# Kernel tuning notes

Measured on AMD Instinct MI355X. Metric: run time of the kernel, lower is better.

The kernel has to match this reference:

```python
import jax, jax.numpy as jnp
import numpy as np
from jax import lax

B, L, V, E, F, C, K = 8, 2500, 50000, 100, 50, 8921, 10
PAD = K // 2  # padding=floor(filter_size/2) -> output length L+1 for even K


def setup_inputs() -> dict:
    key = jax.random.key(0)
    ks = jax.random.split(key, 7)
    text = jax.random.randint(ks[0], (B, L), 0, V, dtype=jnp.int32)
    embed_weight = jax.random.normal(ks[1], (V, E), jnp.float32) * 0.1
    embed_weight = embed_weight.at[0].set(0.0)  # padding_idx=0
    conv_w = jax.random.normal(ks[2], (F, E, K), jnp.float32) * (2.0 / (E * K + F)) ** 0.5
    conv_b = jnp.zeros((F,), jnp.float32)
    Q_w = jax.random.normal(ks[3], (C, F), jnp.float32) * (2.0 / (C + F)) ** 0.5
    out_w = jax.random.normal(ks[4], (C, F), jnp.float32) * (2.0 / (C + F)) ** 0.5
    out_b = jnp.zeros((C,), jnp.float32)
    return {"text": text, "embed_weight": embed_weight, "conv_w": conv_w,
            "conv_b": conv_b, "Q_w": Q_w, "out_w": out_w, "out_b": out_b}


def reference(text, embed_weight, conv_w, conv_b, Q_w, out_w, out_b):
    # Embedding lookup (dropout omitted: eval mode): (B, L, E)
    x = embed_weight[text]
    # Conv1d over length: torch Conv1d(E, F, K, padding=PAD)
    x = jnp.transpose(x, (0, 2, 1))  # (B, E, L)
    z = lax.conv_general_dilated(x, conv_w, window_strides=(1,),
                                 padding=[(PAD, PAD)],
                                 dimension_numbers=("NCH", "OIH", "NCH"))
    z = z + conv_b[None, :, None]
    Z = jnp.tanh(jnp.transpose(z, (0, 2, 1)))  # (B, L', F), L' = L+1
    # Per-label attention: Q_w (C,F) @ Z^T -> (B, C, L'), softmax over length
    scores = jnp.einsum("cf,blf->bcl", Q_w, Z)
    alpha = jax.nn.softmax(scores, axis=2)  # (B, C, L')
    # Attention-weighted sum: (B, C, F)
    Ecf = jnp.einsum("bcl,blf->bcf", alpha, Z)
    # Per-class dot-product readout
    logits = jnp.sum(out_w[None] * Ecf, axis=2) + out_b  # (B, C)
    return logits, alpha
```

## Files before the change

### kernel.cpp

```cpp
#include <hip/hip_runtime.h>
#include <math.h>

#define BB 8
#define LL 2500
#define VV 50000
#define EE 100
#define FF 50
#define CC 8921
#define KK 10
#define PADW 5
#define LOUT 2501
#define NLT 157
#define LPAD (NLT * 16)
#define NCT 140
#define NT16 (NCT * 4)
#define NG 10

typedef __attribute__((ext_vector_type(8))) short bf16x8;
typedef __attribute__((ext_vector_type(4))) float f32x4;

__device__ __forceinline__ short to_bf16(float f) {
  unsigned u = __builtin_bit_cast(unsigned, f);
  u += 0x7FFFu + ((u >> 16) & 1u);
  return (short)(u >> 16);
}

__global__ void k1_conv(const int* __restrict__ text,
                        const float* __restrict__ embed,
                        const float* __restrict__ convw,
                        const float* __restrict__ convb,
                        short* __restrict__ Zp) {
  __shared__ float xw[73 * 101];
  __shared__ short zt[64][72];
  const int b   = blockIdx.y;
  const int l0  = blockIdx.x * 64;
  const int tid = threadIdx.x;

  for (int i = tid; i < 64 * 72 / 2; i += 256) ((int*)zt)[i] = 0;

  for (int idx = tid; idx < 73 * 100; idx += 256) {
    int r = idx / 100;
    int e = idx - r * 100;
    int t = l0 - PADW + r;
    float v = 0.f;
    if (t >= 0 && t < LL) {
      int tok = text[b * LL + t];
      v = embed[tok * EE + e];
    }
    xw[r * 101 + e] = v;
  }
  __syncthreads();

  const int ll = tid & 63;
  const int fg = __builtin_amdgcn_readfirstlane(tid >> 6);
  const int l  = l0 + ll;

  float acc[13];
#pragma unroll
  for (int j = 0; j < 13; ++j) {
    int f = fg + 4 * j;
    acc[j] = (f < FF) ? convb[f] : 0.f;
  }

  for (int e = 0; e < EE; ++e) {
    float xk[KK];
#pragma unroll
    for (int k = 0; k < KK; ++k) xk[k] = xw[(ll + k) * 101 + e];
#pragma unroll
    for (int j = 0; j < 13; ++j) {
      int f = fg + 4 * j;
      if (f < FF) {
        const float* wp = convw + (f * EE + e) * KK;
#pragma unroll
        for (int k = 0; k < KK; ++k) acc[j] += xk[k] * wp[k];
      }
    }
  }

#pragma unroll
  for (int j = 0; j < 13; ++j) {
    int f = fg + 4 * j;
    if (f < FF) {
      float v = (l < LOUT) ? tanhf(acc[j]) : 0.f;
      zt[ll][f] = to_bf16(v);
    }
  }
  __syncthreads();

#pragma unroll
  for (int p = 0; p < 2; ++p) {
    int u    = tid + 256 * p;
    int lane = u & 63, kh = (u >> 6) & 1, i = u >> 7;
    int lt   = blockIdx.x * 4 + i;
    if (lt < NLT) {
      int lrow = i * 16 + (lane & 15);
      int k0   = 4 * (lane >> 4) + 32 * kh;
      uint2 a  = *(const uint2*)&zt[lrow][k0];
      uint2 b2 = *(const uint2*)&zt[lrow][k0 + 16];
      uint4 o; o.x = a.x; o.y = a.y; o.z = b2.x; o.w = b2.y;
      ((uint4*)Zp)[((size_t)b * NLT + lt) * 2 * 64 + kh * 64 + lane] = o;
    }
  }
}

__global__ void k_packW(const float* __restrict__ W, short* __restrict__ Wp) {
  int u = blockIdx.x * 256 + threadIdx.x;
  int lane = u & 63, kh = (u >> 6) & 1, t16 = u >> 7;
  int c  = t16 * 16 + (lane & 15);
  int k0 = 4 * (lane >> 4) + 32 * kh;
  union { short s[8]; uint4 v; } o;
#pragma unroll
  for (int j = 0; j < 8; ++j) {
    int k = k0 + (j & 3) + 16 * (j >> 2);
    float val = (c < CC && k < FF) ? W[c * FF + k] : 0.f;
    o.s[j] = to_bf16(val);
  }
  ((uint4*)Wp)[u] = o.v;
}

__global__ __launch_bounds__(256) void k_attn(
    const short* __restrict__ Zp, const short* __restrict__ Qp,
    const short* __restrict__ Op, const float* __restrict__ outb,
    float* __restrict__ alpha, float* __restrict__ logits) {
  const int id   = blockIdx.x;
  const int b    = id & 7;
  const int ct   = id >> 3;
  const int tid  = threadIdx.x;
  const int w    = tid >> 6;
  const int lane = tid & 63;
  const int g    = lane >> 4, col = lane & 15;
  const int cb   = ct * 64;

  __shared__ float red[4][4][4][4];
  __shared__ float rdinv[64];
  __shared__ float sA[4 * 16 * 68];

  bf16x8 qf[4][2], of[4][2];
#pragma unroll
  for (int mf = 0; mf < 4; ++mf)
#pragma unroll
    for (int kh = 0; kh < 2; ++kh) {
      int t16 = ct * 4 + mf;
      qf[mf][kh] = ((const bf16x8*)Qp)[(t16 * 2 + kh) * 64 + lane];
      of[mf][kh] = ((const bf16x8*)Op)[(t16 * 2 + kh) * 64 + lane];
    }
  const bf16x8* Zb = (const bf16x8*)Zp + (size_t)b * NLT * 2 * 64;

  float dacc[4][4];
#pragma unroll
  for (int mf = 0; mf < 4; ++mf)
#pragma unroll
    for (int r = 0; r < 4; ++r) dacc[mf][r] = 0.f;

  for (int t = 0; t < NG; ++t) {
    const int lt0 = t * 16 + w * 4;
    bf16x8 zz[4][2];
#pragma unroll
    for (int i = 0; i < 4; ++i) {
      int lt = lt0 + i; if (lt > NLT - 1) lt = NLT - 1;
      zz[i][0] = Zb[(lt * 2 + 0) * 64 + lane];
      zz[i][1] = Zb[(lt * 2 + 1) * 64 + lane];
    }
#pragma unroll
    for (int i = 0; i < 4; ++i) {
      int   l    = (lt0 + i) * 16 + col;
      float lmsk = (l < LOUT) ? 1.f : 0.f;
#pragma unroll
      for (int mf = 0; mf < 4; ++mf) {
        f32x4 acc = {0.f, 0.f, 0.f, 0.f};
        acc = __builtin_amdgcn_mfma_f32_16x16x32_bf16(qf[mf][0], zz[i][0], acc, 0, 0, 0);
        acc = __builtin_amdgcn_mfma_f32_16x16x32_bf16(qf[mf][1], zz[i][1], acc, 0, 0, 0);
#pragma unroll
        for (int r = 0; r < 4; ++r) dacc[mf][r] += lmsk * __expf(acc[r]);
      }
    }
  }

#pragma unroll
  for (int mf = 0; mf < 4; ++mf)
#pragma unroll
    for (int r = 0; r < 4; ++r) {
      float v = dacc[mf][r];
      v += __shfl_xor(v, 1); v += __shfl_xor(v, 2);
      v += __shfl_xor(v, 4); v += __shfl_xor(v, 8);
      dacc[mf][r] = v;
    }
  if (col == 0)
#pragma unroll
    for (int mf = 0; mf < 4; ++mf)
#pragma unroll
      for (int r = 0; r < 4; ++r) red[w][mf][g][r] = dacc[mf][r];
  __syncthreads();
  if (tid < 64) {
    int mf = tid >> 4, gg = (tid >> 2) & 3, r = tid & 3;
    float s = red[0][mf][gg][r] + red[1][mf][gg][r] +
              red[2][mf][gg][r] + red[3][mf][gg][r];
    rdinv[tid] = 1.f / s;
  }
  __syncthreads();

  float rd[4][4];
#pragma unroll
  for (int mf = 0; mf < 4; ++mf)
#pragma unroll
    for (int r = 0; r < 4; ++r) rd[mf][r] = rdinv[mf * 16 + g * 4 + r];

  float lacc[4][4];
#pragma unroll
  for (int mf = 0; mf < 4; ++mf)
#pragma unroll
    for (int r = 0; r < 4; ++r) lacc[mf][r] = 0.f;

  float* sAw = sA + w * (16 * 68);

  for (int t = 0; t < NG; ++t) {
    const int lt0 = t * 16 + w * 4;
    bf16x8 zz[4][2];
#pragma unroll
    for (int i = 0; i < 4; ++i) {
      int lt = lt0 + i; if (lt > NLT - 1) lt = NLT - 1;
      zz[i][0] = Zb[(lt * 2 + 0) * 64 + lane];
      zz[i][1] = Zb[(lt * 2 + 1) * 64 + lane];
    }
#pragma unroll
    for (int mf = 0; mf < 4; ++mf) {
#pragma unroll
      for (int i = 0; i < 4; ++i) {
        f32x4 s = {0.f, 0.f, 0.f, 0.f}, tt = {0.f, 0.f, 0.f, 0.f};
        s  = __builtin_amdgcn_mfma_f32_16x16x32_bf16(qf[mf][0], zz[i][0], s, 0, 0, 0);
        s  = __builtin_amdgcn_mfma_f32_16x16x32_bf16(qf[mf][1], zz[i][1], s, 0, 0, 0);
        tt = __builtin_amdgcn_mfma_f32_16x16x32_bf16(of[mf][0], zz[i][0], tt, 0, 0, 0);
        tt = __builtin_amdgcn_mfma_f32_16x16x32_bf16(of[mf][1], zz[i][1], tt, 0, 0, 0);
        int l = (lt0 + i) * 16 + col;
#pragma unroll
        for (int r = 0; r < 4; ++r) {
          float a = __expf(s[r]) * rd[mf][r];
          lacc[mf][r] += (l < LOUT) ? a * tt[r] : 0.f;
          sAw[(g * 4 + r) * 68 + i * 16 + col] = a;
        }
      }
      const int l0w = lt0 * 16;
      const int lw  = l0w + lane;
#pragma unroll
      for (int rr = 0; rr < 16; ++rr) {
        int c = cb + mf * 16 + rr;
        if (lw < LOUT && c < CC)
          __builtin_nontemporal_store(
              sAw[rr * 68 + lane],
              &alpha[(size_t)(b * CC + c) * LOUT + lw]);
      }
    }
  }

#pragma unroll
  for (int mf = 0; mf < 4; ++mf)
#pragma unroll
    for (int r = 0; r < 4; ++r) {
      float v = lacc[mf][r];
      v += __shfl_xor(v, 1); v += __shfl_xor(v, 2);
      v += __shfl_xor(v, 4); v += __shfl_xor(v, 8);
      lacc[mf][r] = v;
    }
  __syncthreads();
  if (col == 0)
#pragma unroll
    for (int mf = 0; mf < 4; ++mf)
#pragma unroll
      for (int r = 0; r < 4; ++r) red[w][mf][g][r] = lacc[mf][r];
  __syncthreads();
  if (tid < 64) {
    int mf = tid >> 4, gg = (tid >> 2) & 3, r = tid & 3;
    int c = cb + tid;
    if (c < CC) {
      float v = red[0][mf][gg][r] + red[1][mf][gg][r] +
                red[2][mf][gg][r] + red[3][mf][gg][r];
      logits[b * CC + c] = v + outb[c];
    }
  }
}

extern "C" void kernel_launch(void* const* d_in, const int* in_sizes, int n_in,
                              void* d_out, int out_size, void* d_ws, size_t ws_size,
                              hipStream_t stream) {
  const int*   text  = (const int*)d_in[0];
  const float* embed = (const float*)d_in[1];
  const float* convw = (const float*)d_in[2];
  const float* convb = (const float*)d_in[3];
  const float* Qw    = (const float*)d_in[4];
  const float* outw  = (const float*)d_in[5];
  const float* outb  = (const float*)d_in[6];

  float* out    = (float*)d_out;
  float* logits = out;
  float* alpha  = out + (size_t)BB * CC;

  short* wsS = (short*)d_ws;
  short* Zp  = wsS;
  short* Qp  = Zp + (size_t)BB * NLT * 2 * 64 * 8;
  short* Op  = Qp + (size_t)NT16 * 2 * 64 * 8;

  k1_conv<<<dim3(40, BB), 256, 0, stream>>>(text, embed, convw, convb, Zp);
  k_packW<<<(NT16 * 128) / 256, 256, 0, stream>>>(Qw, Qp);
  k_packW<<<(NT16 * 128) / 256, 256, 0, stream>>>(outw, Op);
  k_attn<<<dim3(NCT * BB), 256, 0, stream>>>(Zp, Qp, Op, outb, alpha, logits);
}
```

Measured before the change: 672.5 us.

## Split attention into denominator, L-chunked write, and logit-reduce kernels

The single attention kernel becomes three. The first computes the softmax denominators per (batch, class tile) and writes them to a workspace buffer. The second splits the sequence into four chunks per block, which gives four times as many blocks, writes its slice of alpha with 16-byte-grouped stores, and writes partial logits. The third sums the partial logits and adds the bias. The aim is more parallelism and better write coalescing for the large alpha output, at the cost of extra launches and recomputing the score MFMAs in the denominator pass.

```diff
diff --git a/kernel.cpp b/kernel.cpp
--- a/kernel.cpp
+++ b/kernel.cpp
@@ -14,7 +14,8 @@
 #define LPAD (NLT * 16)
 #define NCT 140
 #define NT16 (NCT * 4)
-#define NG 10
+#define NLH 4
+#define CHLT 40
 
 typedef __attribute__((ext_vector_type(8))) short bf16x8;
 typedef __attribute__((ext_vector_type(4))) float f32x4;
@@ -118,10 +119,9 @@
   ((uint4*)Wp)[u] = o.v;
 }
 
-__global__ __launch_bounds__(256) void k_attn(
+__global__ __launch_bounds__(256) void k_attnA(
     const short* __restrict__ Zp, const short* __restrict__ Qp,
-    const short* __restrict__ Op, const float* __restrict__ outb,
-    float* __restrict__ alpha, float* __restrict__ logits) {
+    float* __restrict__ rdinvBuf) {
   const int id   = blockIdx.x;
   const int b    = id & 7;
   const int ct   = id >> 3;
@@ -129,20 +129,16 @@
   const int w    = tid >> 6;
   const int lane = tid & 63;
   const int g    = lane >> 4, col = lane & 15;
-  const int cb   = ct * 64;
 
   __shared__ float red[4][4][4][4];
-  __shared__ float rdinv[64];
-  __shared__ float sA[4 * 16 * 68];
-
-  bf16x8 qf[4][2], of[4][2];
+
+  bf16x8 qf[4][2];
 #pragma unroll
   for (int mf = 0; mf < 4; ++mf)
 #pragma unroll
     for (int kh = 0; kh < 2; ++kh) {
       int t16 = ct * 4 + mf;
       qf[mf][kh] = ((const bf16x8*)Qp)[(t16 * 2 + kh) * 64 + lane];
-      of[mf][kh] = ((const bf16x8*)Op)[(t16 * 2 + kh) * 64 + lane];
     }
   const bf16x8* Zb = (const bf16x8*)Zp + (size_t)b * NLT * 2 * 64;
 
@@ -152,7 +148,7 @@
 #pragma unroll
     for (int r = 0; r < 4; ++r) dacc[mf][r] = 0.f;
 
-  for (int t = 0; t < NG; ++t) {
+  for (int t = 0; t < 10; ++t) {
     const int lt0 = t * 16 + w * 4;
     bf16x8 zz[4][2];
 #pragma unroll
@@ -195,15 +191,54 @@
     int mf = tid >> 4, gg = (tid >> 2) & 3, r = tid & 3;
     float s = red[0][mf][gg][r] + red[1][mf][gg][r] +
               red[2][mf][gg][r] + red[3][mf][gg][r];
-    rdinv[tid] = 1.f / s;
-  }
+    rdinvBuf[(size_t)(b * NCT + ct) * 64 + tid] = 1.f / s;
+  }
+}
+
+__global__ __launch_bounds__(256) void k_attnB(
+    const short* __restrict__ Zp, const short* __restrict__ Qp,
+    const short* __restrict__ Op, const float* __restrict__ rdinvBuf,
+    float* __restrict__ alpha, float* __restrict__ Lpart) {
+  const int id   = blockIdx.x;
+  const int b    = id & 7;
+  const int rest = id >> 3;
+  const int ct   = rest % NCT;
+  const int lh   = rest / NCT;
+  const int tid  = threadIdx.x;
+  const int w    = tid >> 6;
+  const int lane = tid & 63;
+  const int g    = lane >> 4, col = lane & 15;
+  const int cb   = ct * 64;
+  const int q4   = lane >> 4, i16 = lane & 15;
+
+  const int ltStart = lh * CHLT;
+  const int ltEnd   = (ltStart + CHLT < NLT) ? ltStart + CHLT : NLT;
+  const int nLt     = ltEnd - ltStart;
+
+  __shared__ float red[4][4][4][4];
+  __shared__ float rdS[64];
+  __shared__ float sA[4 * 16 * 68];
+  float* sAw = sA + w * (16 * 68);
+
+  if (tid < 64) rdS[tid] = rdinvBuf[(size_t)(b * NCT + ct) * 64 + tid];
+
+  bf16x8 qf[4][2], of[4][2];
+#pragma unroll
+  for (int mf = 0; mf < 4; ++mf)
+#pragma unroll
+    for (int kh = 0; kh < 2; ++kh) {
+      int t16 = ct * 4 + mf;
+      qf[mf][kh] = ((const bf16x8*)Qp)[(t16 * 2 + kh) * 64 + lane];
+      of[mf][kh] = ((const bf16x8*)Op)[(t16 * 2 + kh) * 64 + lane];
+    }
+  const bf16x8* Zb = (const bf16x8*)Zp + (size_t)b * NLT * 2 * 64;
   __syncthreads();
 
   float rd[4][4];
 #pragma unroll
   for (int mf = 0; mf < 4; ++mf)
 #pragma unroll
-    for (int r = 0; r < 4; ++r) rd[mf][r] = rdinv[mf * 16 + g * 4 + r];
+    for (int r = 0; r < 4; ++r) rd[mf][r] = rdS[mf * 16 + g * 4 + r];
 
   float lacc[4][4];
 #pragma unroll
@@ -211,43 +246,60 @@
 #pragma unroll
     for (int r = 0; r < 4; ++r) lacc[mf][r] = 0.f;
 
-  float* sAw = sA + w * (16 * 68);
-
-  for (int t = 0; t < NG; ++t) {
-    const int lt0 = t * 16 + w * 4;
-    bf16x8 zz[4][2];
-#pragma unroll
-    for (int i = 0; i < 4; ++i) {
-      int lt = lt0 + i; if (lt > NLT - 1) lt = NLT - 1;
-      zz[i][0] = Zb[(lt * 2 + 0) * 64 + lane];
-      zz[i][1] = Zb[(lt * 2 + 1) * 64 + lane];
-    }
-#pragma unroll
-    for (int mf = 0; mf < 4; ++mf) {
+  for (int t = 0; t < 3; ++t) {
+    const int lt0r = t * 16 + w * 4;
+    if (lt0r < nLt) {
+      const int lt0 = ltStart + lt0r;
+      bf16x8 zz[4][2];
 #pragma unroll
       for (int i = 0; i < 4; ++i) {
-        f32x4 s = {0.f, 0.f, 0.f, 0.f}, tt = {0.f, 0.f, 0.f, 0.f};
-        s  = __builtin_amdgcn_mfma_f32_16x16x32_bf16(qf[mf][0], zz[i][0], s, 0, 0, 0);
-        s  = __builtin_amdgcn_mfma_f32_16x16x32_bf16(qf[mf][1], zz[i][1], s, 0, 0, 0);
-        tt = __builtin_amdgcn_mfma_f32_16x16x32_bf16(of[mf][0], zz[i][0], tt, 0, 0, 0);
-        tt = __builtin_amdgcn_mfma_f32_16x16x32_bf16(of[mf][1], zz[i][1], tt, 0, 0, 0);
-        int l = (lt0 + i) * 16 + col;
-#pragma unroll
-        for (int r = 0; r < 4; ++r) {
-          float a = __expf(s[r]) * rd[mf][r];
-          lacc[mf][r] += (l < LOUT) ? a * tt[r] : 0.f;
-          sAw[(g * 4 + r) * 68 + i * 16 + col] = a;
+        int lt = lt0 + i; if (lt > NLT - 1) lt = NLT - 1;
+        zz[i][0] = Zb[(lt * 2 + 0) * 64 + lane];
+        zz[i][1] = Zb[(lt * 2 + 1) * 64 + lane];
+      }
+#pragma unroll
+      for (int mf = 0; mf < 4; ++mf) {
+#pragma unroll
+        for (int i = 0; i < 4; ++i) {
+          f32x4 s = {0.f, 0.f, 0.f, 0.f}, tt = {0.f, 0.f, 0.f, 0.f};
+          s  = __builtin_amdgcn_mfma_f32_16x16x32_bf16(qf[mf][0], zz[i][0], s, 0, 0, 0);
+          s  = __builtin_amdgcn_mfma_f32_16x16x32_bf16(qf[mf][1], zz[i][1], s, 0, 0, 0);
+          tt = __builtin_amdgcn_mfma_f32_16x16x32_bf16(of[mf][0], zz[i][0], tt, 0, 0, 0);
+          tt = __builtin_amdgcn_mfma_f32_16x16x32_bf16(of[mf][1], zz[i][1], tt, 0, 0, 0);
+          int l = (lt0 + i) * 16 + col;
+#pragma unroll
+          for (int r = 0; r < 4; ++r) {
+            float a = __expf(s[r]) * rd[mf][r];
+            lacc[mf][r] += (l < LOUT) ? a * tt[r] : 0.f;
+            sAw[(g * 4 + r) * 68 + i * 16 + col] = a;
+          }
         }
-      }
-      const int l0w = lt0 * 16;
-      const int lw  = l0w + lane;
-#pragma unroll
-      for (int rr = 0; rr < 16; ++rr) {
-        int c = cb + mf * 16 + rr;
-        if (lw < LOUT && c < CC)
-          __builtin_nontemporal_store(
-              sAw[rr * 68 + lane],
-              &alpha[(size_t)(b * CC + c) * LOUT + lw]);
+        const int l0w = lt0 * 16;
+        if (l0w + 64 <= LOUT) {
+#pragma unroll
+          for (int s4 = 0; s4 < 4; ++s4) {
+            int rr = s4 * 4 + q4;
+            int c  = cb + mf * 16 + rr;
+            if (c < CC) {
+              f32x4 v = *(const f32x4*)&sAw[rr * 68 + 4 * i16];
+              float* dst = alpha + (size_t)(b * CC + c) * LOUT + l0w + 4 * i16;
+              __builtin_nontemporal_store(v[0], dst + 0);
+              __builtin_nontemporal_store(v[1], dst + 1);
+              __builtin_nontemporal_store(v[2], dst + 2);
+              __builtin_nontemporal_store(v[3], dst + 3);
+            }
+          }
+        } else {
+          const int lw = l0w + lane;
+#pragma unroll
+          for (int rr = 0; rr < 16; ++rr) {
+            int c = cb + mf * 16 + rr;
+            if (lw < LOUT && c < CC)
+              __builtin_nontemporal_store(
+                  sAw[rr * 68 + lane],
+                  &alpha[(size_t)(b * CC + c) * LOUT + lw]);
+          }
+        }
       }
     }
   }
@@ -274,8 +326,21 @@
     if (c < CC) {
       float v = red[0][mf][gg][r] + red[1][mf][gg][r] +
                 red[2][mf][gg][r] + red[3][mf][gg][r];
-      logits[b * CC + c] = v + outb[c];
-    }
+      Lpart[(size_t)lh * (BB * CC) + b * CC + c] = v;
+    }
+  }
+}
+
+__global__ void k_attnC(const float* __restrict__ Lpart,
+                        const float* __restrict__ outb,
+                        float* __restrict__ logits) {
+  int idx = blockIdx.x * 256 + threadIdx.x;
+  if (idx < BB * CC) {
+    int c = idx % CC;
+    float v = outb[c];
+#pragma unroll
+    for (int lh = 0; lh < NLH; ++lh) v += Lpart[(size_t)lh * (BB * CC) + idx];
+    logits[idx] = v;
   }
 }
 
@@ -298,9 +363,14 @@
   short* Zp  = wsS;
   short* Qp  = Zp + (size_t)BB * NLT * 2 * 64 * 8;
   short* Op  = Qp + (size_t)NT16 * 2 * 64 * 8;
+  float* rdinvBuf = (float*)(Op + (size_t)NT16 * 2 * 64 * 8);
+  float* Lpart    = rdinvBuf + (size_t)BB * NCT * 64;
 
   k1_conv<<<dim3(40, BB), 256, 0, stream>>>(text, embed, convw, convb, Zp);
   k_packW<<<(NT16 * 128) / 256, 256, 0, stream>>>(Qw, Qp);
   k_packW<<<(NT16 * 128) / 256, 256, 0, stream>>>(outw, Op);
-  k_attn<<<dim3(NCT * BB), 256, 0, stream>>>(Zp, Qp, Op, outb, alpha, logits);
-}
+  k_attnA<<<dim3(NCT * BB), 256, 0, stream>>>(Zp, Qp, rdinvBuf);
+  k_attnB<<<dim3(NCT * BB * NLH), 256, 0, stream>>>(Zp, Qp, Op, rdinvBuf,
+                                                    alpha, Lpart);
+  k_attnC<<<(BB * CC + 255) / 256, 256, 0, stream>>>(Lpart, outb, logits);
+}
```

Result: no change. 681.1 us (+1.3%).
